# Kernel optimization log

Measured on AMD Instinct MI355X. Metric: run time of the kernel, lower is better.

Reference implementation:

```python
import jax, jax.numpy as jnp
import numpy as np

MAX_TOTAL = 20        # max_total_size
MAX_PER_CLASS = 20    # max_output_size_per_class
SCORE_TH = 0.5        # score_threshold
IOU_TH = 0.5          # tf combined NMS default iou_threshold
K_CAND = 200          # top candidates per class considered for NMS
VARIANCES = jnp.array([0.1, 0.1, 0.2, 0.2], jnp.float32)


def setup_inputs() -> dict:
    key = jax.random.key(0)
    k1, k2, k3, k4, k5, k6 = jax.random.split(key, 6)
    B, N, C = 64, 8732, 21
    pred_deltas = jax.random.normal(k1, (B, N, 4), jnp.float32)
    pred_labels = jax.random.uniform(k2, (B, N, C), dtype=jnp.float32)
    # synthetic normalized anchors (y1,x1,y2,x2) with valid extents
    cy = jax.random.uniform(k3, (N,), dtype=jnp.float32)
    cx = jax.random.uniform(k4, (N,), dtype=jnp.float32)
    h = jax.random.uniform(k5, (N,), dtype=jnp.float32, minval=0.05, maxval=0.3)
    w = jax.random.uniform(k6, (N,), dtype=jnp.float32, minval=0.05, maxval=0.3)
    anchors = jnp.stack([cy - h / 2, cx - w / 2, cy + h / 2, cx + w / 2], axis=-1)
    return {"pred_deltas": pred_deltas, "pred_labels": pred_labels, "anchors": anchors}


def _decode(anchors, deltas):
    # anchors [N,4] (y1,x1,y2,x2); deltas [B,N,4] (dy,dx,dh,dw) -> boxes [B,N,4]
    ah = anchors[:, 2] - anchors[:, 0]
    aw = anchors[:, 3] - anchors[:, 1]
    acy = anchors[:, 0] + 0.5 * ah
    acx = anchors[:, 1] + 0.5 * aw
    cy = deltas[..., 0] * ah + acy
    cx = deltas[..., 1] * aw + acx
    h = jnp.exp(deltas[..., 2]) * ah
    w = jnp.exp(deltas[..., 3]) * aw
    return jnp.stack([cy - 0.5 * h, cx - 0.5 * w, cy + 0.5 * h, cx + 0.5 * w], axis=-1)


def _pairwise_iou(boxes):
    # boxes [K,4] -> iou [K,K]
    y1, x1, y2, x2 = boxes[:, 0], boxes[:, 1], boxes[:, 2], boxes[:, 3]
    area = (y2 - y1) * (x2 - x1)
    ih = jnp.clip(jnp.minimum(y2[:, None], y2[None, :]) - jnp.maximum(y1[:, None], y1[None, :]), 0.0)
    iw = jnp.clip(jnp.minimum(x2[:, None], x2[None, :]) - jnp.maximum(x1[:, None], x1[None, :]), 0.0)
    inter = ih * iw
    return inter / (area[:, None] + area[None, :] - inter + 1e-8)


def _nms_one_class(scores, boxes):
    # scores [N], boxes [N,4] -> (top scores [MAX_PER_CLASS], boxes [MAX_PER_CLASS,4])
    vals, idx = jax.lax.top_k(scores, K_CAND)          # sorted desc
    cboxes = boxes[idx]                                # [K,4]
    iou = _pairwise_iou(cboxes)                        # [K,K]
    valid = vals > SCORE_TH
    ar = jnp.arange(K_CAND)

    def body(i, keep):
        suppressed = jnp.any(keep & (iou[i] > IOU_TH) & (ar < i))
        return keep.at[i].set(valid[i] & ~suppressed)

    keep = jax.lax.fori_loop(0, K_CAND, body, jnp.zeros(K_CAND, dtype=bool))
    kept_scores = jnp.where(keep, vals, 0.0)
    top_vals, top_i = jax.lax.top_k(kept_scores, MAX_PER_CLASS)
    return top_vals, cboxes[top_i]


def reference(pred_deltas, pred_labels, anchors):
    deltas = pred_deltas * VARIANCES                       # variance scaling
    boxes = _decode(anchors, deltas)                       # [B,N,4]
    # zero out all class scores where argmax class == 0 (background)
    lab_map = jnp.argmax(pred_labels, axis=-1, keepdims=True)
    scores = jnp.where(lab_map != 0, pred_labels, 0.0)     # [B,N,C]

    per_class = jax.vmap(_nms_one_class, in_axes=(1, None))   # over classes
    per_batch = jax.vmap(per_class, in_axes=(0, 0))           # over batch
    cls_scores, cls_boxes = per_batch(scores, boxes)          # [B,C,P], [B,C,P,4]

    B, C, P = cls_scores.shape
    flat_scores = cls_scores.reshape(B, C * P)
    flat_boxes = cls_boxes.reshape(B, C * P, 4)
    class_ids = jnp.broadcast_to(jnp.arange(C, dtype=jnp.float32)[:, None], (C, P)).reshape(-1)

    top_vals, top_i = jax.lax.top_k(flat_scores, MAX_TOTAL)   # [B,MAX_TOTAL]
    final_boxes = jnp.take_along_axis(flat_boxes, top_i[..., None], axis=1)
    final_boxes = jnp.clip(final_boxes, 0.0, 1.0)             # combined NMS clip_boxes=True
    valid = top_vals > 0.0
    final_boxes = jnp.where(valid[..., None], final_boxes, 0.0)
    final_labels = jnp.where(valid, class_ids[top_i], 0.0)
    return final_boxes, top_vals, final_labels
```

## Files before the change

kernel.cpp:

```cpp
#include <hip/hip_runtime.h>
#include <stdint.h>

typedef unsigned long long u64;
typedef unsigned int u32;
typedef unsigned short u16;

#define BATCH 64
#define NANCH 8732
#define NCHUNK 1092
#define NCLS 21
#define KCAND 200
#define CAP 2048
#define PPC 20
#define PTOT 20
#define PRETHR 0.9f

__global__ __launch_bounds__(256) void kzero(u32* __restrict__ cnt)
{
    int i = blockIdx.x * 256 + threadIdx.x;
    if (i < BATCH * NCLS) cnt[i] = 0;
}

__global__ __launch_bounds__(256) void kdecode(
    const float* __restrict__ labels,
    unsigned char* __restrict__ msk, u64* __restrict__ lists,
    u32* __restrict__ cnt, int useT)
{
#pragma clang fp contract(off)
    const int n = blockIdx.x * 256 + threadIdx.x;
    const int b = blockIdx.y;
    const int lane = threadIdx.x & 63;
    const bool active = (n < NANCH);

    float v[NCLS];
#pragma unroll
    for (int c = 0; c < NCLS; ++c) v[c] = 0.0f;
    bool mk = false;
    if (active) {
        const float* lab = labels + ((size_t)b * NANCH + n) * NCLS;
#pragma unroll
        for (int c = 0; c < NCLS; ++c) v[c] = lab[c];
        float mx = v[0]; int am = 0;
#pragma unroll
        for (int c = 1; c < NCLS; ++c) if (v[c] > mx) { mx = v[c]; am = c; }
        mk = (am != 0);
        msk[(size_t)b * NANCH + n] = mk ? 1 : 0;
    }
    if (!useT) return;

    u32 myHits = 0;
#pragma unroll
    for (int c = 0; c < NCLS; ++c)
        if (active && mk && v[c] >= PRETHR) myHits |= (1u << c);

    u32 myCnt = 0;
#pragma unroll
    for (int c = 0; c < NCLS; ++c) {
        u64 m = __ballot((myHits >> c) & 1u);
        if (lane == c) myCnt = (u32)__popcll(m);
    }
    u32 myBase = 0;
    if (lane < NCLS) myBase = atomicAdd(&cnt[b * NCLS + lane], myCnt);

#pragma unroll
    for (int c = 0; c < NCLS; ++c) {
        u64 m = __ballot((myHits >> c) & 1u);
        u32 base = (u32)__shfl((int)myBase, c, 64);
        if ((m >> lane) & 1ull) {
            u32 rank = (u32)__popcll(m & ((1ull << lane) - 1ull));
            u32 slot = base + rank;
            if (slot < CAP)
                lists[((size_t)b * NCLS + c) * CAP + slot] =
                    ((u64)__float_as_uint(v[c]) << 32) | (u32)(~(u32)n);
        }
    }
}

__device__ __forceinline__ u64 shflxor64(u64 x, int m) {
    return (u64)__shfl_xor((long long)x, m, 64);
}

__device__ __forceinline__ void suffixFind(const u32* hist, u32* waveTot, int nb, int need,
                                           int* sSel, int* sAbove, int* sH, int* sTot,
                                           int tid, int lane, int wv)
{
    int K = (nb + 255) >> 8;
    int base = tid * K;
    u32 own = 0;
    for (int q = 0; q < K; ++q) { int bi = base + q; own += (bi < nb) ? hist[bi] : 0u; }
    u32 s = own;
#pragma unroll
    for (int d = 1; d < 64; d <<= 1) {
        u32 o = __shfl_down(s, d, 64);
        if (lane + d < 64) s += o;
    }
    if (lane == 0) waveTot[wv] = s;
    __syncthreads();
    if (tid == 0 && sTot) *sTot = (int)(waveTot[0] + waveTot[1] + waveTot[2] + waveTot[3]);
    u32 add = 0;
    for (int w = wv + 1; w < 4; ++w) add += waveTot[w];
    u32 cum = (s - own) + add;
    for (int q = K - 1; q >= 0; --q) {
        int bi = base + q;
        u32 hh = (bi < nb) ? hist[bi] : 0u;
        if (cum < (u32)need && cum + hh >= (u32)need) { *sSel = bi; *sAbove = (int)cum; *sH = (int)hh; }
        cum += hh;
    }
    __syncthreads();
}

__global__ __launch_bounds__(256) void knms(
    const float* __restrict__ labels, const unsigned char* __restrict__ msk,
    const u64* __restrict__ lists, const u32* __restrict__ cnt,
    const float* __restrict__ deltas, const float* __restrict__ anchors,
    float* __restrict__ clsScores, float* __restrict__ clsBoxes, int useT)
{
#pragma clang fp contract(off)
    __shared__ __align__(16) char smem[8192];
    u32*   hist = (u32*)smem;
    float* cbY1 = (float*)smem;
    float* cbX1 = (float*)(smem + 1024);
    float* cbY2 = (float*)(smem + 2048);
    float* cbX2 = (float*)(smem + 3072);
    float* cbAr = (float*)(smem + 4096);
    float* cVal = (float*)(smem + 5120);
    u64*   iouT = (u64*)(smem + 6144);
    __shared__ u64 candKey[256];
    __shared__ u32 waveTot[4];
    __shared__ float outS[PPC];
    __shared__ float outB[PPC * 4];
    __shared__ int sSel, sAbove, sH, sTot, sN, sKP;

    const int tid = threadIdx.x;
    const int lane = tid & 63;
    const int wv = tid >> 6;
    const int bc = blockIdx.x;
    const int b = bc / NCLS;
    const int c = bc % NCLS;

    const int nTHR = useT ? (int)cnt[bc] : -1;
    const bool fast = useT && (nTHR >= KCAND) && (nTHR <= CAP);

    if (fast) {
        const u64* lst = lists + (size_t)bc * CAP;
        u64 kr[8];
#pragma unroll
        for (int q = 0; q < 8; ++q) {
            int i = q * 256 + tid;
            kr[q] = (i < nTHR) ? lst[i] : 0ull;
        }
        for (int q = tid; q < 1024; q += 256) hist[1024 + q] = 0;
        if (tid == 0) { sSel = -1; sAbove = 0; sH = 0; sN = 0; sKP = 0; }
        __syncthreads();
#pragma unroll
        for (int q = 0; q < 8; ++q) {
            if (q * 256 + tid < nTHR) {
                float v = __uint_as_float((u32)(kr[q] >> 32));
                u32 t = (u32)(v * 65536.0f);
                atomicAdd(&hist[t >> 5], 1u);
            }
        }
        __syncthreads();
        suffixFind(hist + 1024, waveTot, 1024, KCAND, &sSel, &sAbove, &sH, nullptr, tid, lane, wv);
        int A = sAbove;
        u32 T16 = (u32)(1024 + sSel) << 5;
        int cnt2 = A + sH;

        if (cnt2 > 256) {
            if (tid < 32) hist[tid] = 0;
            if (tid == 0) { sSel = -1; sAbove = 0; sH = 0; }
            __syncthreads();
#pragma unroll
            for (int q = 0; q < 8; ++q) {
                if (q * 256 + tid < nTHR) {
                    float v = __uint_as_float((u32)(kr[q] >> 32));
                    u32 t = (u32)(v * 65536.0f);
                    if (t >= T16 && t < T16 + 32) atomicAdd(&hist[t - T16], 1u);
                }
            }
            __syncthreads();
            suffixFind(hist, waveTot, 32, KCAND - A, &sSel, &sAbove, &sH, nullptr, tid, lane, wv);
            A += sAbove;
            T16 += (u32)sSel;
        }
#pragma unroll
        for (int q = 0; q < 8; ++q) {
            if (q * 256 + tid < nTHR) {
                float v = __uint_as_float((u32)(kr[q] >> 32));
                u32 t = (u32)(v * 65536.0f);
                if (t >= T16) {
                    int slot = atomicAdd(&sN, 1);
                    if (slot < 256) candKey[slot] = kr[q];
                }
            }
        }
    } else {
        uint4 rc[5];
        for (int q = 0; q < 5; ++q) {
            int chunk = q * 256 + tid;
            u32 w4[4] = {0, 0, 0, 0};
            if (chunk < NCHUNK) {
                for (int w = 0; w < 4; ++w)
                    for (int h = 0; h < 2; ++h) {
                        int n = chunk * 8 + w * 2 + h;
                        u32 t = 0;
                        if (n < NANCH && msk[(size_t)b * NANCH + n]) {
                            float v = labels[((size_t)b * NANCH + n) * NCLS + c];
                            t = (u32)(v * 65536.0f);
                        }
                        w4[w] |= t << (16 * h);
                    }
            }
            rc[q] = make_uint4(w4[0], w4[1], w4[2], w4[3]);
        }
        for (int q = tid; q < 1024; q += 256) hist[1024 + q] = 0;
        if (tid == 0) { sSel = -1; sAbove = 0; sH = 0; sTot = 0; sN = 0; sKP = 0; }
        __syncthreads();
#pragma unroll
        for (int q = 0; q < 5; ++q) {
            if (q * 256 + tid < NCHUNK) {
                u32 w4[4] = {rc[q].x, rc[q].y, rc[q].z, rc[q].w};
#pragma unroll
                for (int w = 0; w < 4; ++w) {
                    u32 lo = w4[w] & 0xFFFFu, hi = w4[w] >> 16;
                    if (lo & 0x8000u) atomicAdd(&hist[lo >> 5], 1u);
                    if (hi & 0x8000u) atomicAdd(&hist[hi >> 5], 1u);
                }
            }
        }
        __syncthreads();
        suffixFind(hist + 1024, waveTot, 1024, KCAND, &sSel, &sAbove, &sH, &sTot, tid, lane, wv);
        int A; int cnt2; u32 T16;
        if (sTot < KCAND) { T16 = 32768u; A = 0; cnt2 = sTot; }
        else { A = sAbove; T16 = (u32)(1024 + sSel) << 5; cnt2 = A + sH; }
        if (cnt2 > 256) {
            if (tid < 32) hist[tid] = 0;
            if (tid == 0) { sSel = -1; sAbove = 0; sH = 0; }
            __syncthreads();
#pragma unroll
            for (int q = 0; q < 5; ++q) {
                if (q * 256 + tid < NCHUNK) {
                    u32 w4[4] = {rc[q].x, rc[q].y, rc[q].z, rc[q].w};
#pragma unroll
                    for (int w = 0; w < 4; ++w) {
                        u32 lo = w4[w] & 0xFFFFu, hi = w4[w] >> 16;
                        if (lo >= T16 && lo < T16 + 32) atomicAdd(&hist[lo - T16], 1u);
                        if (hi >= T16 && hi < T16 + 32) atomicAdd(&hist[hi - T16], 1u);
                    }
                }
            }
            __syncthreads();
            suffixFind(hist, waveTot, 32, KCAND - A, &sSel, &sAbove, &sH, nullptr, tid, lane, wv);
            A += sAbove;
            T16 += (u32)sSel;
        }
#pragma unroll
        for (int q = 0; q < 5; ++q) {
            int chunk = q * 256 + tid;
            if (chunk < NCHUNK) {
                u32 w4[4] = {rc[q].x, rc[q].y, rc[q].z, rc[q].w};
#pragma unroll
                for (int w = 0; w < 4; ++w) {
#pragma unroll
                    for (int h = 0; h < 2; ++h) {
                        u32 t = (h == 0) ? (w4[w] & 0xFFFFu) : (w4[w] >> 16);
                        if (t >= T16) {
                            int n = chunk * 8 + w * 2 + h;
                            float v = labels[((size_t)b * NANCH + n) * NCLS + c];
                            int slot = atomicAdd(&sN, 1);
                            if (slot < 256)
                                candKey[slot] = ((u64)__float_as_uint(v) << 32) | (u32)(~(u32)n);
                        }
                    }
                }
            }
        }
    }
    __syncthreads();
    int nc = sN; if (nc > 256) nc = 256;

    u64 x = (tid < nc) ? candKey[tid] : 0ull;
    for (int k = 2; k <= 256; k <<= 1) {
        for (int j = k >> 1; j > 0; j >>= 1) {
            u64 y;
            if (j < 64) {
                y = shflxor64(x, j);
            } else {
                __syncthreads();
                candKey[tid] = x;
                __syncthreads();
                y = candKey[tid ^ j];
            }
            bool keepMax = ((tid & k) == 0) == ((tid & j) == 0);
            u64 mx = (x > y) ? x : y;
            u64 mn = (x > y) ? y : x;
            x = keepMax ? mx : mn;
        }
    }

    float myV = __uint_as_float((u32)(x >> 32));
    float myY1 = 0.f, myX1 = 0.f, myY2 = 0.f, myX2 = 0.f, myAr = 0.f;
    u32 idx = ~(u32)x;
    if (tid < KCAND && idx < (u32)NANCH) {
        float4 d = ((const float4*)deltas)[(size_t)b * NANCH + idx];
        float4 a = ((const float4*)anchors)[idx];
        float ah = a.z - a.x, aw = a.w - a.y;
        float acy = a.x + 0.5f * ah, acx = a.y + 0.5f * aw;
        float cy = (d.x * 0.1f) * ah + acy;
        float cx = (d.y * 0.1f) * aw + acx;
        float hh2 = expf(d.z * 0.2f) * ah;
        float ww2 = expf(d.w * 0.2f) * aw;
        myY1 = cy - 0.5f * hh2; myX1 = cx - 0.5f * ww2;
        myY2 = cy + 0.5f * hh2; myX2 = cx + 0.5f * ww2;
        myAr = (myY2 - myY1) * (myX2 - myX1);
    } else {
        myV = 0.f;
    }
    __syncthreads();
    cbY1[tid] = myY1; cbX1[tid] = myX1; cbY2[tid] = myY2; cbX2[tid] = myX2;
    cbAr[tid] = myAr; cVal[tid] = myV;

    u64 k0 = 0, k1 = 0, k2 = 0, k3 = 0;
    int KPw = 0;
    for (int t0 = 0; t0 < 4; ++t0) {
        __syncthreads();
        if (sKP >= PPC) break;
        int rowBase = t0 * 64;
        int rows = KCAND - rowBase; if (rows > 64) rows = 64;
        for (int r = wv; r < rows; r += 4) {
            int i = rowBase + r;
            float y1i = cbY1[i], x1i = cbX1[i], y2i = cbY2[i], x2i = cbX2[i], ari = cbAr[i];
            for (int cg = 0; cg <= t0; ++cg) {
                int j = cg * 64 + lane;
                float ih = fminf(y2i, cbY2[j]) - fmaxf(y1i, cbY1[j]);
                ih = fmaxf(ih, 0.0f);
                float iw = fminf(x2i, cbX2[j]) - fmaxf(x1i, cbX1[j]);
                iw = fmaxf(iw, 0.0f);
                float inter = ih * iw;
                float iou = inter / (ari + cbAr[j] - inter + 1e-8f);
                u64 bal = __ballot(iou > 0.5f);
                if (lane == 0) iouT[r * 4 + cg] = bal;
            }
        }
        __syncthreads();
        if (tid < 64) {
            int i = rowBase + lane;
            u64 r0 = 0, r1 = 0, r2 = 0, r3 = 0;
            bool vld = false;
            if (lane < rows) {
                r0 = iouT[lane * 4 + 0]; r1 = iouT[lane * 4 + 1];
                r2 = iouT[lane * 4 + 2]; r3 = iouT[lane * 4 + 3];
                vld = cVal[i] > 0.5f;
            }
            for (int l = 0; l < rows; ++l) {
                int mydec = (vld && !((k0 & r0) | (k1 & r1) | (k2 & r2) | (k3 & r3))) ? 1 : 0;
                int d = __shfl(mydec, l, 64);
                if (d) {
                    u64 bit = 1ull << l;
                    if (t0 == 0) k0 |= bit; else if (t0 == 1) k1 |= bit;
                    else if (t0 == 2) k2 |= bit; else k3 |= bit;
                    ++KPw;
                    if (KPw >= PPC) break;
                }
            }
            if (tid == 0) sKP = KPw;
        }
    }
    __syncthreads();

    if (tid < PPC) outS[tid] = 0.0f;
    if (tid < PPC * 4) outB[tid] = 0.0f;
    __syncthreads();

    if (tid < 64) {
        int base = 0;
#pragma unroll
        for (int chunk = 0; chunk < 4; ++chunk) {
            u64 kw = (chunk == 0) ? k0 : (chunk == 1) ? k1 : (chunk == 2) ? k2 : k3;
            int i = chunk * 64 + tid;
            bool kept = ((kw >> tid) & 1ull) != 0;
            int rank = base + (int)__popcll(kw & ((1ull << tid) - 1ull));
            if (kept && rank < PPC && i < KCAND) {
                outS[rank] = cVal[i];
                outB[rank * 4 + 0] = cbY1[i];
                outB[rank * 4 + 1] = cbX1[i];
                outB[rank * 4 + 2] = cbY2[i];
                outB[rank * 4 + 3] = cbX2[i];
            }
            base += (int)__popcll(kw);
        }
    }
    __syncthreads();
    if (tid < PPC) clsScores[(size_t)bc * PPC + tid] = outS[tid];
    if (tid < PPC * 4) clsBoxes[(size_t)bc * PPC * 4 + tid] = outB[tid];
}

__global__ __launch_bounds__(512) void kmerge(
    const float* __restrict__ clsScores, const float* __restrict__ clsBoxes,
    float* __restrict__ out)
{
#pragma clang fp contract(off)
    __shared__ u64 key[512];
    const int tid = threadIdx.x;
    const int b = blockIdx.x;
    const int F = NCLS * PPC;
    u64 kk = 0;
    if (tid < F) {
        float v = clsScores[(size_t)b * F + tid];
        kk = ((u64)__float_as_uint(v) << 32) | (u32)(~(u32)tid);
    }
    key[tid] = kk;
    for (int k = 2; k <= 512; k <<= 1)
        for (int j = k >> 1; j > 0; j >>= 1) {
            __syncthreads();
            int ixj = tid ^ j;
            if (ixj > tid) {
                u64 a = key[tid], bb = key[ixj];
                if (((tid & k) == 0) ? (a < bb) : (a > bb)) { key[tid] = bb; key[ixj] = a; }
            }
        }
    __syncthreads();
    if (tid < PTOT) {
        u64 kx = key[tid];
        float v = __uint_as_float((u32)(kx >> 32));
        u32 f = ~((u32)kx);
        bool valid = (v > 0.0f) && (f < (u32)F);
        float cls = valid ? (float)(f / PPC) : 0.0f;
        float* oB = out;
        float* oV = out + (size_t)BATCH * PTOT * 4;
        float* oL = oV + (size_t)BATCH * PTOT;
#pragma unroll
        for (int q = 0; q < 4; ++q) {
            float xq = 0.0f;
            if (valid) {
                xq = clsBoxes[((size_t)b * F + f) * 4 + q];
                xq = fminf(fmaxf(xq, 0.0f), 1.0f);
            }
            oB[((size_t)b * PTOT + tid) * 4 + q] = xq;
        }
        oV[(size_t)b * PTOT + tid] = v;
        oL[(size_t)b * PTOT + tid] = cls;
    }
}

extern "C" void kernel_launch(void* const* d_in, const int* in_sizes, int n_in,
                              void* d_out, int out_size, void* d_ws, size_t ws_size,
                              hipStream_t stream)
{
    const float* deltas  = (const float*)d_in[0];
    const float* labels  = (const float*)d_in[1];
    const float* anchors = (const float*)d_in[2];
    float* out = (float*)d_out;
    char* ws = (char*)d_ws;

    const size_t mskOff  = 0;
    const size_t cntOff  = 558848;
    const size_t csOff   = 564480;
    const size_t cbOff   = 672000;
    const size_t listOff = 1102336;
    const size_t needT   = 23122432;

    unsigned char* msk = (unsigned char*)(ws + mskOff);
    u32* cnt         = (u32*)(ws + cntOff);
    float* clsScores = (float*)(ws + csOff);
    float* clsBoxes  = (float*)(ws + cbOff);
    u64* lists       = (u64*)(ws + listOff);
    int useT = (ws_size >= needT) ? 1 : 0;

    if (useT) kzero<<<(BATCH * NCLS + 255) / 256, 256, 0, stream>>>(cnt);
    dim3 gA((NANCH + 255) / 256, BATCH);
    kdecode<<<gA, 256, 0, stream>>>(labels, msk, lists, cnt, useT);
    knms<<<BATCH * NCLS, 256, 0, stream>>>(labels, msk, lists, cnt, deltas, anchors,
                                           clsScores, clsBoxes, useT);
    kmerge<<<BATCH, 512, 0, stream>>>(clsScores, clsBoxes, out);
}
```

Baseline: 58.55 us.

## Shrink NMS histogram window, aggregate atomics per wave, shuffle-based merge sort

The fast path's first-level histogram now covers only the bins from HWIN upward (256 bins instead of 1024), since keys are all above the 0.9 pre-threshold. This cuts the zeroing and the suffix scan. Candidate compaction uses a wave ballot with one atomic per wave instead of one per thread. The merge kernel's bitonic sort uses 64-bit cross-lane shuffles for strides under 64 and shared memory only for larger strides, which removes most barriers. The zero kernel is replaced with hipMemsetAsync. The window assumes no score maps below bin 1792, and slot ordering among candidates changes.

```diff
diff --git a/kernel.cpp b/kernel.cpp
--- a/kernel.cpp
+++ b/kernel.cpp
@@ -14,12 +14,7 @@
 #define PPC 20
 #define PTOT 20
 #define PRETHR 0.9f
-
-__global__ __launch_bounds__(256) void kzero(u32* __restrict__ cnt)
-{
-    int i = blockIdx.x * 256 + threadIdx.x;
-    if (i < BATCH * NCLS) cnt[i] = 0;
-}
+#define HWIN 1792
 
 __global__ __launch_bounds__(256) void kdecode(
     const float* __restrict__ labels,
@@ -149,7 +144,7 @@
             int i = q * 256 + tid;
             kr[q] = (i < nTHR) ? lst[i] : 0ull;
         }
-        for (int q = tid; q < 1024; q += 256) hist[1024 + q] = 0;
+        hist[tid] = 0;
         if (tid == 0) { sSel = -1; sAbove = 0; sH = 0; sN = 0; sKP = 0; }
         __syncthreads();
 #pragma unroll
@@ -157,13 +152,13 @@
             if (q * 256 + tid < nTHR) {
                 float v = __uint_as_float((u32)(kr[q] >> 32));
                 u32 t = (u32)(v * 65536.0f);
-                atomicAdd(&hist[t >> 5], 1u);
-            }
-        }
-        __syncthreads();
-        suffixFind(hist + 1024, waveTot, 1024, KCAND, &sSel, &sAbove, &sH, nullptr, tid, lane, wv);
+                atomicAdd(&hist[(t >> 5) - HWIN], 1u);
+            }
+        }
+        __syncthreads();
+        suffixFind(hist, waveTot, 256, KCAND, &sSel, &sAbove, &sH, nullptr, tid, lane, wv);
         int A = sAbove;
-        u32 T16 = (u32)(1024 + sSel) << 5;
+        u32 T16 = (u32)(HWIN + sSel) << 5;
         int cnt2 = A + sH;
 
         if (cnt2 > 256) {
@@ -185,11 +180,19 @@
         }
 #pragma unroll
         for (int q = 0; q < 8; ++q) {
-            if (q * 256 + tid < nTHR) {
+            int i = q * 256 + tid;
+            bool pred = (i < nTHR);
+            if (pred) {
                 float v = __uint_as_float((u32)(kr[q] >> 32));
-                u32 t = (u32)(v * 65536.0f);
-                if (t >= T16) {
-                    int slot = atomicAdd(&sN, 1);
+                pred = ((u32)(v * 65536.0f) >= T16);
+            }
+            u64 m = __ballot(pred);
+            if (m) {
+                int base = 0;
+                if (lane == 0) base = atomicAdd(&sN, (int)__popcll(m));
+                base = __shfl(base, 0, 64);
+                if (pred) {
+                    int slot = base + (int)__popcll(m & ((1ull << lane) - 1ull));
                     if (slot < 256) candKey[slot] = kr[q];
                 }
             }
@@ -404,26 +407,31 @@
     const int tid = threadIdx.x;
     const int b = blockIdx.x;
     const int F = NCLS * PPC;
-    u64 kk = 0;
+    u64 x = 0;
     if (tid < F) {
         float v = clsScores[(size_t)b * F + tid];
-        kk = ((u64)__float_as_uint(v) << 32) | (u32)(~(u32)tid);
-    }
-    key[tid] = kk;
-    for (int k = 2; k <= 512; k <<= 1)
-        for (int j = k >> 1; j > 0; j >>= 1) {
-            __syncthreads();
-            int ixj = tid ^ j;
-            if (ixj > tid) {
-                u64 a = key[tid], bb = key[ixj];
-                if (((tid & k) == 0) ? (a < bb) : (a > bb)) { key[tid] = bb; key[ixj] = a; }
-            }
-        }
-    __syncthreads();
+        x = ((u64)__float_as_uint(v) << 32) | (u32)(~(u32)tid);
+    }
+    for (int k = 2; k <= 512; k <<= 1) {
+        for (int j = k >> 1; j >= 1; j >>= 1) {
+            u64 y;
+            if (j < 64) {
+                y = shflxor64(x, j);
+            } else {
+                __syncthreads();
+                key[tid] = x;
+                __syncthreads();
+                y = key[tid ^ j];
+            }
+            bool keepMax = ((tid & k) == 0) == ((tid & j) == 0);
+            u64 mx = x > y ? x : y;
+            u64 mn = x > y ? y : x;
+            x = keepMax ? mx : mn;
+        }
+    }
     if (tid < PTOT) {
-        u64 kx = key[tid];
-        float v = __uint_as_float((u32)(kx >> 32));
-        u32 f = ~((u32)kx);
+        float v = __uint_as_float((u32)(x >> 32));
+        u32 f = ~((u32)x);
         bool valid = (v > 0.0f) && (f < (u32)F);
         float cls = valid ? (float)(f / PPC) : 0.0f;
         float* oB = out;
@@ -467,7 +475,7 @@
     u64* lists       = (u64*)(ws + listOff);
     int useT = (ws_size >= needT) ? 1 : 0;
 
-    if (useT) kzero<<<(BATCH * NCLS + 255) / 256, 256, 0, stream>>>(cnt);
+    if (useT) hipMemsetAsync(cnt, 0, BATCH * NCLS * sizeof(u32), stream);
     dim3 gA((NANCH + 255) / 256, BATCH);
     kdecode<<<gA, 256, 0, stream>>>(labels, msk, lists, cnt, useT);
     knms<<<BATCH * NCLS, 256, 0, stream>>>(labels, msk, lists, cnt, deltas, anchors,
```

Result: no change. 58.43 us (-0.2%).
